# Kernel tuning notes

Measured on AMD Instinct MI355X. Metric: run time of the kernel, lower is better.

The kernel has to match this reference:

```python
import jax, jax.numpy as jnp
import numpy as np

N_NODES = 50000
N_EDGES = 200000
HID = 32
EDGE_DIM = 16
EDGE_HIDDEN = 128


def setup_inputs() -> dict:
    key = jax.random.key(0)
    ks = jax.random.split(key, 10)
    nf = jax.random.normal(ks[0], (N_NODES, HID), dtype=jnp.float32)
    ef = jax.random.normal(ks[1], (N_EDGES, EDGE_DIM), dtype=jnp.float32)
    edge_src = jax.random.randint(ks[2], (N_EDGES,), 0, N_NODES, dtype=jnp.int32)
    edge_dst = jax.random.randint(ks[3], (N_EDGES,), 0, N_NODES, dtype=jnp.int32)
    # edge_func MLP: EDGE_DIM -> EDGE_HIDDEN -> HID*HID (per-edge weight matrix)
    s1 = 1.0 / np.sqrt(EDGE_DIM)
    s2 = 1.0 / np.sqrt(EDGE_HIDDEN)
    W1 = jax.random.uniform(ks[4], (EDGE_DIM, EDGE_HIDDEN), jnp.float32, -s1, s1)
    b1 = jax.random.uniform(ks[5], (EDGE_HIDDEN,), jnp.float32, -s1, s1)
    W2 = jax.random.uniform(ks[6], (EDGE_HIDDEN, HID * HID), jnp.float32, -s2, s2)
    b2 = jax.random.uniform(ks[7], (HID * HID,), jnp.float32, -s2, s2)
    bias = jnp.zeros((HID,), dtype=jnp.float32)  # NNConv output bias
    return {"nf": nf, "ef": ef, "edge_src": edge_src, "edge_dst": edge_dst,
            "W1": W1, "b1": b1, "W2": W2, "b2": b2, "bias": bias}


def reference(nf, ef, edge_src, edge_dst, W1, b1, W2, b2, bias):
    # edge network: per-edge weight matrix [E, HID, HID]
    h = jax.nn.relu(ef @ W1 + b1)
    We = (h @ W2 + b2).reshape(-1, HID, HID)
    # gather source features, per-edge matvec message [E, HID]
    msg = jnp.einsum('ei,eio->eo', nf[edge_src], We)
    # sum-aggregate messages at destination nodes, add bias
    agg = jax.ops.segment_sum(msg, edge_dst, num_segments=nf.shape[0])
    return agg + bias
```

## Files before the change

### kernel.cpp

```cpp
#include <hip/hip_runtime.h>


#define E_TOTAL   200000
#define N_NODES   50000
#define TILES     3125
#define OUT_BLKS  6250
#define W2K_BLKS  512
#define NBLK      256
#define NTL_BIG   53
#define LDS_BYTES 159744

typedef short short8  __attribute__((ext_vector_type(8)));
typedef float f32x16  __attribute__((ext_vector_type(16)));

__device__ __forceinline__ short f2bf(float f) {
    union { float f; unsigned u; } cv; cv.f = f;
    unsigned r = cv.u + 0x7fffu + ((cv.u >> 16) & 1u);
    return (short)(r >> 16);
}

__device__ __forceinline__ void gll16(const short* gsrc, short* ldst) {
    __builtin_amdgcn_global_load_lds(
        (const __attribute__((address_space(1))) unsigned int*)gsrc,
        (__attribute__((address_space(3))) unsigned int*)ldst, 16, 0, 0);
}

__global__ __launch_bounds__(256) void setup_kernel(const float* __restrict__ W2,
                                                    const float* __restrict__ bias,
                                                    float* __restrict__ out,
                                                    short* __restrict__ W2p) {
    int bid = blockIdx.x, tid = threadIdx.x;
    if (bid < OUT_BLKS) {
        int i = bid * 256 + tid;
        out[i] = bias[i & 31];
    } else {
        int g = (bid - OUT_BLKS) * 256 + tid;
        int k = g >> 10, ci = g & 1023;
        int i = ci >> 5, o = ci & 31;
        int p = o >> 4, o15 = o & 15;
        int c = i * 16 + o15;
        int ks = k >> 4, kl = k & 15;
        int idx = p * 65536 + ks * 8192 + (c >> 5) * 512 + (kl >> 3) * 256 + (c & 31) * 8 + (kl & 7);
        W2p[idx] = f2bf(W2[g]);
    }
}

__global__ __launch_bounds__(512, 2) void mpnn_kernel(const float* __restrict__ nf,
                                                      const float* __restrict__ ef,
                                                      const int*   __restrict__ esrc,
                                                      const int*   __restrict__ edst,
                                                      const float* __restrict__ W1,
                                                      const float* __restrict__ b1,
                                                      const float* __restrict__ b2,
                                                      const short* __restrict__ W2p,
                                                      float* __restrict__ out) {
    extern __shared__ __align__(16) unsigned char smem[];
    short* W2s  = (short*)(smem);
    short* W1Ts = (short*)(smem + 131072);
    short* Hs   = (short*)(smem + 135168);
    float* Xs   = (float*)(smem + 151552);
    float* pbuf = (float*)(smem + 135168);

    const int tid = threadIdx.x;
    const int w   = tid >> 6;
    const int l31 = tid & 31;
    const int lh  = (tid >> 5) & 1;
    const int o15 = l31 & 15;
    const int ib  = l31 >> 4;
    const int bid = blockIdx.x;
    const int ntl = (bid < NTL_BIG) ? 13 : 12;
    const int itn = 2 * ntl;

    float4 xreg; short8 efreg;
    float  b2v0, b2v1;
    {
        #pragma unroll
        for (int j = 0; j < 16; ++j)
            gll16(W2p + w * 8192 + j * 512 + (tid & 63) * 8, W2s + w * 8192 + j * 512);
    }
    {
        int g = tid * 4; int i = g >> 7; int c0 = g & 127;
        float4 v = *(const float4*)(W1 + g);
        float vv[4] = {v.x, v.y, v.z, v.w};
        #pragma unroll
        for (int u = 0; u < 4; ++u) {
            int c = c0 + u;
            W1Ts[c * 16 + (((i >> 3) ^ ((c >> 2) & 1)) << 3) + (i & 7)] = f2bf(vv[u]);
        }
    }
    {
        int s = esrc[bid * 64 + (tid >> 3)];
        xreg = *(const float4*)(nf + (size_t)s * 32 + (tid & 7) * 4);
        int eL = l31 + ((w & 1) << 5);
        const float* ep = ef + (size_t)(bid * 64 + eL) * 16 + lh * 8;
        float4 a0 = *(const float4*)(ep);
        float4 a1 = *(const float4*)(ep + 4);
        efreg[0] = f2bf(a0.x); efreg[1] = f2bf(a0.y); efreg[2] = f2bf(a0.z); efreg[3] = f2bf(a0.w);
        efreg[4] = f2bf(a1.x); efreg[5] = f2bf(a1.y); efreg[6] = f2bf(a1.z); efreg[7] = f2bf(a1.w);
    }
    b2v0 = b2[(4 * w + ib) * 32 + o15];
    b2v1 = b2[(4 * w + 2 + ib) * 32 + o15];
    const int   cW1  = ((w >> 1) << 5) + l31;
    const float b1v  = b1[cW1];

    __syncthreads();
    const short8 w1frag = *(const short8*)(W1Ts + cW1 * 16 + ((lh ^ ((cW1 >> 2) & 1)) << 3));

    for (int it = 0; it < itn; ++it) {
        const int pass = (it >= ntl) ? 1 : 0;
        const int tile = bid + (it - pass * ntl) * NBLK;
        const int ebase = tile * 64;

        if (it == ntl) {
            #pragma unroll
            for (int j = 0; j < 16; ++j)
                gll16(W2p + 65536 + w * 8192 + j * 512 + (tid & 63) * 8, W2s + w * 8192 + j * 512);
            b2v0 = b2[(4 * w + ib) * 32 + 16 + o15];
            b2v1 = b2[(4 * w + 2 + ib) * 32 + 16 + o15];
        }
        __syncthreads();

        *(float4*)(Xs + (tid >> 3) * 32 + (tid & 7) * 4) = xreg;

        {
            f32x16 hacc;
            #pragma unroll
            for (int q = 0; q < 16; ++q) hacc[q] = 0.f;
            hacc = __builtin_amdgcn_mfma_f32_32x32x16_bf16(efreg, w1frag, hacc, 0, 0, 0);
            const int mh = w & 1, G1 = cW1 >> 3, j1 = cW1 & 7;
            #pragma unroll
            for (int r = 0; r < 16; ++r) {
                int ee = (r & 3) + ((r >> 2) << 3) + (lh << 2) + (mh << 5);
                float v = fmaxf(hacc[r] + b1v, 0.f);
                Hs[G1 * 512 + ((ee ^ (G1 & 7)) << 3) + j1] = f2bf(v);
            }
        }
        __syncthreads();

        int nit = it + 1; if (nit >= itn) nit = it;
        const int npass = (nit >= ntl) ? 1 : 0;
        const int nebase = (bid + (nit - npass * ntl) * NBLK) * 64;

        f32x16 acc00, acc01, acc10, acc11;
        #pragma unroll
        for (int q = 0; q < 16; ++q) { acc00[q] = 0.f; acc01[q] = 0.f; acc10[q] = 0.f; acc11[q] = 0.f; }
        int pre_s = 0;
        #pragma unroll
        for (int ks = 0; ks < 8; ++ks) {
            const int G  = 2 * ks + lh;
            const int ax = ((l31 ^ (G & 7)) << 3);
            short8 afr0 = *(const short8*)(Hs + G * 512 + ax);
            short8 afr1 = *(const short8*)(Hs + G * 512 + ax + 256);
            short8 bfr0 = *(const short8*)(W2s + ks * 8192 + (2 * w    ) * 512 + lh * 256 + l31 * 8);
            short8 bfr1 = *(const short8*)(W2s + ks * 8192 + (2 * w + 1) * 512 + lh * 256 + l31 * 8);
            acc00 = __builtin_amdgcn_mfma_f32_32x32x16_bf16(afr0, bfr0, acc00, 0, 0, 0);
            acc01 = __builtin_amdgcn_mfma_f32_32x32x16_bf16(afr1, bfr0, acc01, 0, 0, 0);
            acc10 = __builtin_amdgcn_mfma_f32_32x32x16_bf16(afr0, bfr1, acc10, 0, 0, 0);
            acc11 = __builtin_amdgcn_mfma_f32_32x32x16_bf16(afr1, bfr1, acc11, 0, 0, 0);
            if (ks == 1) pre_s = esrc[nebase + (tid >> 3)];
            if (ks == 3) {
                int eL = l31 + ((w & 1) << 5);
                const float* ep = ef + (size_t)(nebase + eL) * 16 + lh * 8;
                float4 a0 = *(const float4*)(ep);
                float4 a1 = *(const float4*)(ep + 4);
                efreg[0] = f2bf(a0.x); efreg[1] = f2bf(a0.y); efreg[2] = f2bf(a0.z); efreg[3] = f2bf(a0.w);
                efreg[4] = f2bf(a1.x); efreg[5] = f2bf(a1.y); efreg[6] = f2bf(a1.z); efreg[7] = f2bf(a1.w);
            }
            if (ks == 5) xreg = *(const float4*)(nf + (size_t)pre_s * 32 + (tid & 7) * 4);
        }

        float sv0[16], sv1[16];
        #pragma unroll
        for (int r = 0; r < 16; ++r) {
            int e0 = (r & 3) + ((r >> 2) << 3) + (lh << 2);
            float4 xv = *(const float4*)(Xs + e0 * 32 + 4 * w);
            float xa = ib ? xv.y : xv.x;
            float xb = ib ? xv.w : xv.z;
            float v = xa * (acc00[r] + b2v0) + xb * (acc10[r] + b2v1);
            v += __shfl_xor(v, 16);
            sv0[r] = v;
            float4 xw = *(const float4*)(Xs + (e0 + 32) * 32 + 4 * w);
            float xc = ib ? xw.y : xw.x;
            float xd = ib ? xw.w : xw.z;
            float v1 = xc * (acc01[r] + b2v0) + xd * (acc11[r] + b2v1);
            v1 += __shfl_xor(v1, 16);
            sv1[r] = v1;
        }

        __syncthreads();
        if (w < 4) {
            #pragma unroll
            for (int r = 0; r < 16; ++r) {
                int e = (r & 3) + ((r >> 2) << 3) + (lh << 2) + (ib << 5);
                pbuf[(w << 10) + (e << 4) + o15] = ib ? sv1[r] : sv0[r];
            }
        }
        __syncthreads();
        if (w >= 4) {
            #pragma unroll
            for (int r = 0; r < 16; ++r) {
                int e = (r & 3) + ((r >> 2) << 3) + (lh << 2) + (ib << 5);
                pbuf[((w - 4) << 10) + (e << 4) + o15] += ib ? sv1[r] : sv0[r];
            }
        }
        __syncthreads();
        #pragma unroll
        for (int p2 = 0; p2 < 2; ++p2) {
            int idx = tid + (p2 << 9);
            float v = pbuf[idx] + pbuf[idx + 1024] + pbuf[idx + 2048] + pbuf[idx + 3072];
            int e = idx >> 4, oo = idx & 15;
            int d = edst[ebase + e];
            atomicAdd(out + (size_t)d * 32 + (pass << 4) + oo, v);
        }
    }
}

extern "C" void kernel_launch(void* const* d_in, const int* in_sizes, int n_in,
                              void* d_out, int out_size, void* d_ws, size_t ws_size,
                              hipStream_t stream) {
    const float* nf   = (const float*)d_in[0];
    const float* ef   = (const float*)d_in[1];
    const int*   src  = (const int*)  d_in[2];
    const int*   dst  = (const int*)  d_in[3];
    const float* W1   = (const float*)d_in[4];
    const float* b1   = (const float*)d_in[5];
    const float* W2   = (const float*)d_in[6];
    const float* b2   = (const float*)d_in[7];
    const float* bias = (const float*)d_in[8];
    float* out = (float*)d_out;
    short* W2p = (short*)d_ws;

    static bool init_done = false;
    if (!init_done) {
        hipFuncSetAttribute((const void*)mpnn_kernel,
                            hipFuncAttributeMaxDynamicSharedMemorySize, LDS_BYTES);
        init_done = true;
    }

    setup_kernel<<<OUT_BLKS + W2K_BLKS, 256, 0, stream>>>(W2, bias, out, W2p);
    mpnn_kernel<<<NBLK, 512, LDS_BYTES, stream>>>(nf, ef, src, dst, W1, b1, b2, W2p, out);
}
```

Before: 191.3 us.

## Defer scatter atomics into next tile's MFMA loop, vectorize setup, swizzle pbuf

The atomicAdd scatter of each tile's reduced messages is deferred and issued during the next tile's MFMA loop, so atomic latency overlaps with compute. The last tile's atomics are flushed after the loop. The setup kernel now writes the bias-initialised output with float4 stores and builds the packed bf16 W2 with one 16-byte store per thread instead of scattered 2-byte writes. The partial-sum buffer gets an XOR swizzle to cut LDS bank conflicts, and X values are read as scalars instead of float4 plus select. The deferral costs extra live registers, and the scalar LDS reads add load instructions.

Result: faster. 184.5 us (-3.5%).

```diff
diff --git a/kernel.cpp b/kernel.cpp
--- a/kernel.cpp
+++ b/kernel.cpp
@@ -4,8 +4,9 @@
 #define E_TOTAL   200000
 #define N_NODES   50000
 #define TILES     3125
-#define OUT_BLKS  6250
-#define W2K_BLKS  512
+#define OUT4      400000
+#define OUT4_BLKS 1563
+#define W2C_BLKS  64
 #define NBLK      256
 #define NTL_BIG   53
 #define LDS_BYTES 159744
@@ -30,18 +31,25 @@
                                                     float* __restrict__ out,
                                                     short* __restrict__ W2p) {
     int bid = blockIdx.x, tid = threadIdx.x;
-    if (bid < OUT_BLKS) {
-        int i = bid * 256 + tid;
-        out[i] = bias[i & 31];
+    if (bid < OUT4_BLKS) {
+        int i4 = bid * 256 + tid;
+        if (i4 < OUT4) {
+            float4 bv = *(const float4*)(bias + ((i4 & 7) << 2));
+            *(float4*)(out + (size_t)i4 * 4) = bv;
+        }
     } else {
-        int g = (bid - OUT_BLKS) * 256 + tid;
-        int k = g >> 10, ci = g & 1023;
-        int i = ci >> 5, o = ci & 31;
-        int p = o >> 4, o15 = o & 15;
-        int c = i * 16 + o15;
-        int ks = k >> 4, kl = k & 15;
-        int idx = p * 65536 + ks * 8192 + (c >> 5) * 512 + (kl >> 3) * 256 + (c & 31) * 8 + (kl & 7);
-        W2p[idx] = f2bf(W2[g]);
+        int q = (bid - OUT4_BLKS) * 256 + tid;
+        int p  = q >> 13;
+        int ch = q & 8191;
+        int ks = ch >> 10, ct = (ch >> 6) & 15, lhg = (ch >> 5) & 1, cc = ch & 31;
+        int c  = ct * 32 + cc;
+        int i  = c >> 4, o15 = c & 15;
+        int ci = i * 32 + p * 16 + o15;
+        int kb = ks * 16 + lhg * 8;
+        short8 pk;
+        #pragma unroll
+        for (int j = 0; j < 8; ++j) pk[j] = f2bf(W2[(size_t)(kb + j) * 1024 + ci]);
+        *(short8*)(W2p + (size_t)q * 8) = pk;
     }
 }
 
@@ -67,6 +75,7 @@
     const int lh  = (tid >> 5) & 1;
     const int o15 = l31 & 15;
     const int ib  = l31 >> 4;
+    const int xbw = lh ^ ib;
     const int bid = blockIdx.x;
     const int ntl = (bid < NTL_BIG) ? 13 : 12;
     const int itn = 2 * ntl;
@@ -105,6 +114,9 @@
 
     __syncthreads();
     const short8 w1frag = *(const short8*)(W1Ts + cW1 * 16 + ((lh ^ ((cW1 >> 2) & 1)) << 3));
+
+    float  pv0 = 0.f, pv1 = 0.f;
+    float *pa0 = out, *pa1 = out;
 
     for (int it = 0; it < itn; ++it) {
         const int pass = (it >= ntl) ? 1 : 0;
@@ -158,6 +170,10 @@
             acc10 = __builtin_amdgcn_mfma_f32_32x32x16_bf16(afr0, bfr1, acc10, 0, 0, 0);
             acc11 = __builtin_amdgcn_mfma_f32_32x32x16_bf16(afr1, bfr1, acc11, 0, 0, 0);
             if (ks == 1) pre_s = esrc[nebase + (tid >> 3)];
+            if (ks == 2 && it > 0) {
+                atomicAdd(pa0, pv0);
+                atomicAdd(pa1, pv1);
+            }
             if (ks == 3) {
                 int eL = l31 + ((w & 1) << 5);
                 const float* ep = ef + (size_t)(nebase + eL) * 16 + lh * 8;
@@ -169,19 +185,18 @@
             if (ks == 5) xreg = *(const float4*)(nf + (size_t)pre_s * 32 + (tid & 7) * 4);
         }
 
+        const int xc0 = 4 * w + ib, xc1 = 4 * w + 2 + ib;
         float sv0[16], sv1[16];
         #pragma unroll
         for (int r = 0; r < 16; ++r) {
             int e0 = (r & 3) + ((r >> 2) << 3) + (lh << 2);
-            float4 xv = *(const float4*)(Xs + e0 * 32 + 4 * w);
-            float xa = ib ? xv.y : xv.x;
-            float xb = ib ? xv.w : xv.z;
+            float xa = Xs[e0 * 32 + xc0];
+            float xb = Xs[e0 * 32 + xc1];
             float v = xa * (acc00[r] + b2v0) + xb * (acc10[r] + b2v1);
             v += __shfl_xor(v, 16);
             sv0[r] = v;
-            float4 xw = *(const float4*)(Xs + (e0 + 32) * 32 + 4 * w);
-            float xc = ib ? xw.y : xw.x;
-            float xd = ib ? xw.w : xw.z;
+            float xc = Xs[(e0 + 32) * 32 + xc0];
+            float xd = Xs[(e0 + 32) * 32 + xc1];
             float v1 = xc * (acc01[r] + b2v0) + xd * (acc11[r] + b2v1);
             v1 += __shfl_xor(v1, 16);
             sv1[r] = v1;
@@ -192,7 +207,7 @@
             #pragma unroll
             for (int r = 0; r < 16; ++r) {
                 int e = (r & 3) + ((r >> 2) << 3) + (lh << 2) + (ib << 5);
-                pbuf[(w << 10) + (e << 4) + o15] = ib ? sv1[r] : sv0[r];
+                pbuf[(w << 10) + ((e ^ xbw) << 4) + o15] = ib ? sv1[r] : sv0[r];
             }
         }
         __syncthreads();
@@ -200,19 +215,27 @@
             #pragma unroll
             for (int r = 0; r < 16; ++r) {
                 int e = (r & 3) + ((r >> 2) << 3) + (lh << 2) + (ib << 5);
-                pbuf[((w - 4) << 10) + (e << 4) + o15] += ib ? sv1[r] : sv0[r];
-            }
-        }
-        __syncthreads();
-        #pragma unroll
-        for (int p2 = 0; p2 < 2; ++p2) {
-            int idx = tid + (p2 << 9);
-            float v = pbuf[idx] + pbuf[idx + 1024] + pbuf[idx + 2048] + pbuf[idx + 3072];
+                pbuf[((w - 4) << 10) + ((e ^ xbw) << 4) + o15] += ib ? sv1[r] : sv0[r];
+            }
+        }
+        __syncthreads();
+        {
+            int idx = tid;
             int e = idx >> 4, oo = idx & 15;
-            int d = edst[ebase + e];
-            atomicAdd(out + (size_t)d * 32 + (pass << 4) + oo, v);
-        }
-    }
+            int xbE = ((e >> 2) ^ (e >> 5)) & 1;
+            int a = ((e ^ xbE) << 4) + oo;
+            pv0 = pbuf[a] + pbuf[a + 1024] + pbuf[a + 2048] + pbuf[a + 3072];
+            pa0 = out + (size_t)edst[ebase + e] * 32 + (pass << 4) + oo;
+            idx = tid + 512;
+            e = idx >> 4; oo = idx & 15;
+            xbE = ((e >> 2) ^ (e >> 5)) & 1;
+            a = ((e ^ xbE) << 4) + oo;
+            pv1 = pbuf[a] + pbuf[a + 1024] + pbuf[a + 2048] + pbuf[a + 3072];
+            pa1 = out + (size_t)edst[ebase + e] * 32 + (pass << 4) + oo;
+        }
+    }
+    atomicAdd(pa0, pv0);
+    atomicAdd(pa1, pv1);
 }
 
 extern "C" void kernel_launch(void* const* d_in, const int* in_sizes, int n_in,
@@ -237,6 +260,6 @@
         init_done = true;
     }
 
-    setup_kernel<<<OUT_BLKS + W2K_BLKS, 256, 0, stream>>>(W2, bias, out, W2p);
+    setup_kernel<<<OUT4_BLKS + W2C_BLKS, 256, 0, stream>>>(W2, bias, out, W2p);
     mpnn_kernel<<<NBLK, 512, LDS_BYTES, stream>>>(nf, ef, src, dst, W1, b1, b2, W2p, out);
 }
```
